# Optimization experiments

Hardware: AMD Instinct MI355X
Metric: run time of the kernel (lower is better)

## Reference

```python
import jax, jax.numpy as jnp
import numpy as np

B, N, D = 32, 4096, 256      # batch, num input features, input dim
S, H, M = 11, 256, 512       # num_slots, slot_size, mlp_hidden_size
ITERS = 3
ATTN_EPS = 1e-8
LN_EPS = 1e-5


def layer_norm(x, scale, offset):
    mu = jnp.mean(x, axis=-1, keepdims=True)
    var = jnp.var(x, axis=-1, keepdims=True)
    return (x - mu) * scale * jax.lax.rsqrt(var + LN_EPS) + offset


def gru_unroll(updates, w_i, w_h, b):
    # haiku hk.GRU unrolled over axis 1 (time_major=False), zero initial state.
    # updates: [B, T, H]
    h0 = jnp.zeros((updates.shape[0], H), updates.dtype)
    def step(h, x):
        gx = jnp.matmul(x, w_i)                                    # [B, 3H]
        zr = jax.nn.sigmoid(gx[:, :2 * H] + jnp.matmul(h, w_h[:, :2 * H]) + b[:2 * H])
        z, r = zr[:, :H], zr[:, H:]
        a = jnp.tanh(gx[:, 2 * H:] + jnp.matmul(r * h, w_h[:, 2 * H:]) + b[2 * H:])
        h_new = (1.0 - z) * h + z * a
        return h_new, h_new
    _, outs = jax.lax.scan(step, h0, jnp.swapaxes(updates, 0, 1))
    return jnp.swapaxes(outs, 0, 1)                                # [B, T, H]


def setup_inputs():
    key = jax.random.key(0)
    k = jax.random.split(key, 16)
    def lin(kk, fan_in, fan_out):
        return jax.random.normal(kk, (fan_in, fan_out), jnp.float32) / np.sqrt(fan_in).astype(np.float32)
    return {
        "inputs": jax.random.normal(k[0], (B, N, D), jnp.float32),
        "slot_noise": jax.random.normal(k[1], (B, S, H), jnp.float32),
        "ln_in_scale": jnp.ones((D,), jnp.float32),
        "ln_in_offset": jnp.zeros((D,), jnp.float32),
        "ln_slots_scale": jnp.ones((H,), jnp.float32),
        "ln_slots_offset": jnp.zeros((H,), jnp.float32),
        "ln_mlp_scale": jnp.ones((H,), jnp.float32),
        "ln_mlp_offset": jnp.zeros((H,), jnp.float32),
        "slots_mu": jax.random.normal(k[2], (1, 1, H), jnp.float32) * 0.1,
        "slots_log_sigma": jax.random.normal(k[3], (1, 1, H), jnp.float32) * 0.1 - 1.0,
        "Wq": lin(k[4], H, H),
        "Wk": lin(k[5], D, H),
        "Wv": lin(k[6], D, H),
        "gru_wi": lin(k[7], H, 3 * H),
        "gru_wh": lin(k[8], H, 3 * H),
        "gru_b": jnp.zeros((3 * H,), jnp.float32),
        "mlp_w1": lin(k[9], H, M),
        "mlp_b1": jnp.zeros((M,), jnp.float32),
        "mlp_w2": lin(k[10], M, H),
        "mlp_b2": jnp.zeros((H,), jnp.float32),
    }


def reference(inputs, slot_noise, ln_in_scale, ln_in_offset, ln_slots_scale,
              ln_slots_offset, ln_mlp_scale, ln_mlp_offset, slots_mu,
              slots_log_sigma, Wq, Wk, Wv, gru_wi, gru_wh, gru_b,
              mlp_w1, mlp_b1, mlp_w2, mlp_b2):
    x = layer_norm(inputs, ln_in_scale, ln_in_offset)
    kf = jnp.matmul(x, Wk)                                          # [B, N, H]
    vf = jnp.matmul(x, Wv)                                          # [B, N, H]
    slots = slots_mu + jnp.exp(slots_log_sigma) * slot_noise        # [B, S, H]
    scale = H ** (-0.5)
    for _ in range(ITERS):
        q = jnp.matmul(layer_norm(slots, ln_slots_scale, ln_slots_offset), Wq) * scale
        attn_logits = jnp.einsum('bnh,bsh->bns', kf, q)             # [B, N, S]
        attn = jax.nn.softmax(attn_logits, axis=-1) + ATTN_EPS      # softmax over slots
        attn = attn / jnp.sum(attn, axis=-2, keepdims=True)         # normalize over inputs
        updates = jnp.einsum('bns,bnh->bsh', attn, vf)              # [B, S, H]
        slots = gru_unroll(updates, gru_wi, gru_wh, gru_b)          # GRU over slot axis
        mlp_in = layer_norm(slots, ln_mlp_scale, ln_mlp_offset)
        hid = jax.nn.relu(jnp.matmul(mlp_in, mlp_w1) + mlp_b1)
        slots = slots + jnp.matmul(hid, mlp_w2) + mlp_b2
    return slots
```

## Files before the change

kernel.cpp:

```cpp
#include <hip/hip_runtime.h>

typedef unsigned short u16;
typedef __bf16 bf16x8 __attribute__((ext_vector_type(8)));
typedef float  f32x4  __attribute__((ext_vector_type(4)));
typedef unsigned short u16x8 __attribute__((ext_vector_type(8)));

union U8cast { u16x8 u; bf16x8 b; };

#define NB 32
#define NN 4096
#define ND 256
#define NS 11
#define NH 256
#define NM 512

__device__ __forceinline__ u16 f2bf(float f) {
  unsigned u = __float_as_uint(f);
  u += 0x7FFF + ((u >> 16) & 1);
  return (u16)(u >> 16);
}
__device__ __forceinline__ float bf2f(u16 h) {
  return __uint_as_float(((unsigned)h) << 16);
}

__device__ __forceinline__ void gload_lds16(const void* g, void* l) {
  __builtin_amdgcn_global_load_lds((const __attribute__((address_space(1))) void*)g,
                                   (__attribute__((address_space(3))) void*)l, 16, 0, 0);
}

__global__ void k_stats_ln(const float* __restrict__ x, const float* __restrict__ sc,
                           const float* __restrict__ of, u16* __restrict__ xbf) {
  int lane = threadIdx.x & 63;
  int wid  = threadIdx.x >> 6;
  int row  = blockIdx.x * 4 + wid;
  float4 v = *(const float4*)(x + (size_t)row * 256 + lane * 4);
  float s1 = v.x + v.y + v.z + v.w;
  float s2 = v.x*v.x + v.y*v.y + v.z*v.z + v.w*v.w;
#pragma unroll
  for (int off = 32; off; off >>= 1) { s1 += __shfl_xor(s1, off); s2 += __shfl_xor(s2, off); }
  float mu = s1 * (1.f/256.f);
  float rs = rsqrtf(s2 * (1.f/256.f) - mu*mu + 1e-5f);
  float4 s4 = *(const float4*)(sc + lane * 4);
  float4 o4 = *(const float4*)(of + lane * 4);
  ushort4 o;
  o.x = f2bf((v.x - mu) * (rs * s4.x) + o4.x);
  o.y = f2bf((v.y - mu) * (rs * s4.y) + o4.y);
  o.z = f2bf((v.z - mu) * (rs * s4.z) + o4.z);
  o.w = f2bf((v.w - mu) * (rs * s4.w) + o4.w);
  *(ushort4*)(xbf + (size_t)row * 256 + lane * 4) = o;
}

__global__ __launch_bounds__(256)
void k_cvt_w(const float* __restrict__ Wk, const float* __restrict__ Wv,
             u16* __restrict__ wT) {
  __shared__ float Lt[64][65];
  int bx = blockIdx.x;
  int kt = bx & 3, ct = bx >> 2;
  int k0 = kt * 64, c0 = ct * 64;
  const float* src = (c0 < 256) ? Wk : Wv;
  int c0m = c0 & 255;
  int t = threadIdx.x;
  int kr = t >> 2, part = t & 3;
  const float* sp = src + (size_t)(k0 + kr) * 256 + c0m + part * 16;
#pragma unroll
  for (int g = 0; g < 4; ++g) {
    float4 v = *(const float4*)(sp + g * 4);
    Lt[kr][part*16 + g*4 + 0] = v.x;
    Lt[kr][part*16 + g*4 + 1] = v.y;
    Lt[kr][part*16 + g*4 + 2] = v.z;
    Lt[kr][part*16 + g*4 + 3] = v.w;
  }
  __syncthreads();
  int cr = t >> 2;
  u16* wp = wT + (size_t)(c0 + cr) * 256 + k0 + part * 16;
#pragma unroll
  for (int g = 0; g < 2; ++g) {
    u16x8 o;
#pragma unroll
    for (int j = 0; j < 8; ++j) o[j] = f2bf(Lt[part*16 + g*8 + j][cr]);
    *(u16x8*)(wp + g * 8) = o;
  }
}

__global__ __launch_bounds__(256)
void k_mk(const float* __restrict__ Wq, const u16* __restrict__ wT,
          u16* __restrict__ Mb) {
  __shared__ float xn[256];
  __shared__ float part[8][256];
  int e = blockIdx.x, t = threadIdx.x;
  xn[t] = Wq[e*256 + t];
  __syncthreads();
  int tc = t & 31, kg = t >> 5;
  float a[8] = {};
#pragma unroll 8
  for (int kk = 0; kk < 32; ++kk) {
    int k = kg*32 + kk;
    float xv = xn[k];
    u16x8 wv = *(const u16x8*)(wT + k*256 + tc*8);
#pragma unroll
    for (int j = 0; j < 8; ++j) a[j] += xv * bf2f(wv[j]);
  }
  *(float4*)&part[kg][tc*8]     = make_float4(a[0], a[1], a[2], a[3]);
  *(float4*)&part[kg][tc*8 + 4] = make_float4(a[4], a[5], a[6], a[7]);
  __syncthreads();
  float s = 0.f;
#pragma unroll
  for (int g = 0; g < 8; ++g) s += part[g][t];
  Mb[e*256 + t] = f2bf(s);
}

__global__ void k_cvt_all(const float* __restrict__ wi, const float* __restrict__ wh,
                          const float* __restrict__ w1, const float* __restrict__ w2,
                          const float* __restrict__ noise, const float* __restrict__ smu,
                          const float* __restrict__ sls,
                          u16* __restrict__ wib, u16* __restrict__ whb,
                          u16* __restrict__ w1b, u16* __restrict__ w2b,
                          float* __restrict__ slots) {
  int idx = blockIdx.x * 256 + threadIdx.x;
  if      (idx < 196608) wib[idx]          = f2bf(wi[idx]);
  else if (idx < 393216) whb[idx - 196608] = f2bf(wh[idx - 196608]);
  else if (idx < 524288) w1b[idx - 393216] = f2bf(w1[idx - 393216]);
  else if (idx < 655360) w2b[idx - 524288] = f2bf(w2[idx - 524288]);
  else {
    int i = idx - 655360;
    int c = i & 255;
    slots[i] = smu[c] + expf(sls[c]) * noise[i];
  }
}

__global__ __launch_bounds__(256)
void k_gemm_vf(const u16* __restrict__ xbf, const u16* __restrict__ wTv,
               u16* __restrict__ vf) {
  __shared__ __align__(16) u16 Al[2][128 * 64];
  __shared__ __align__(16) u16 Bl[2][128 * 64];
  int t = threadIdx.x;
  int bid = blockIdx.x;
  int xcd  = bid & 7;
  int slot = bid >> 3;
  int colt = slot & 1;
  int rowt = xcd * 128 + (slot >> 1);
  int row0 = rowt * 128;
  int col0 = colt * 128;

  int lane = t & 63, w = t >> 6;
  int wm = (w & 1) * 64, wn = (w >> 1) * 64;
  int fr = lane & 15, kq = lane >> 4;

  int srow = w * 8 + (lane >> 3);
  int k2   = (((lane & 7) ^ ((lane >> 3) & 7)) << 4);
  const u16* agp = xbf + (size_t)(row0 + srow) * 256 + (k2 >> 1);
  const u16* bgp = wTv + (size_t)(col0 + srow) * 256 + (k2 >> 1);

  f32x4 acc[4][4] = {};

#define STAGE_VF(buf, kc)                                              \
  {                                                                    \
    u16* Aw = &Al[buf][w * 512];                                       \
    u16* Bw = &Bl[buf][w * 512];                                       \
    _Pragma("unroll")                                                  \
    for (int i = 0; i < 4; ++i) {                                      \
      gload_lds16(agp + (size_t)i * 32 * 256 + (kc), Aw + i * 2048);   \
      gload_lds16(bgp + (size_t)i * 32 * 256 + (kc), Bw + i * 2048);   \
    }                                                                  \
  }

  STAGE_VF(0, 0);
  __syncthreads();
#pragma unroll
  for (int t4 = 0; t4 < 4; ++t4) {
    if (t4 < 3) STAGE_VF((t4 + 1) & 1, (t4 + 1) * 64);
    const u16* Ab = Al[t4 & 1];
    const u16* Bb = Bl[t4 & 1];
#pragma unroll
    for (int ks = 0; ks < 2; ++ks) {
      int kb = ks * 64 + kq * 16;
      bf16x8 af[4], bfr[4];
#pragma unroll
      for (int i = 0; i < 4; ++i) {
        int row = wm + i * 16 + fr;
        af[i] = *(const bf16x8*)((const char*)Ab + row * 128 + (kb ^ ((fr & 7) << 4)));
      }
#pragma unroll
      for (int i = 0; i < 4; ++i) {
        int row = wn + i * 16 + fr;
        bfr[i] = *(const bf16x8*)((const char*)Bb + row * 128 + (kb ^ ((fr & 7) << 4)));
      }
#pragma unroll
      for (int im = 0; im < 4; ++im)
#pragma unroll
        for (int in = 0; in < 4; ++in)
          acc[im][in] = __builtin_amdgcn_mfma_f32_16x16x32_bf16(af[im], bfr[in], acc[im][in], 0, 0, 0);
    }
    __syncthreads();
  }
#undef STAGE_VF

  int r4 = kq * 4;
#pragma unroll
  for (int im = 0; im < 4; ++im)
#pragma unroll
    for (int in = 0; in < 4; ++in) {
      int gcol = col0 + wn + in*16 + fr;
#pragma unroll
      for (int r = 0; r < 4; ++r) {
        int grow = row0 + wm + im*16 + r4 + r;
        vf[(size_t)grow * 256 + gcol] = f2bf(acc[im][in][r]);
      }
    }
}

__global__ __launch_bounds__(256)
void k_q_ln(const float* __restrict__ slots, const float* __restrict__ sc,
            const float* __restrict__ of, const u16* __restrict__ Mb,
            float* __restrict__ qk2, float* __restrict__ updates,
            float* __restrict__ colsum) {
  __shared__ float xn[256];
  __shared__ float red[8];
  __shared__ float part[8][256];
  int row = blockIdx.x, t = threadIdx.x;
  float v = slots[row*256 + t];
  float s1 = v, s2 = v*v;
#pragma unroll
  for (int off = 32; off; off >>= 1) { s1 += __shfl_xor(s1, off); s2 += __shfl_xor(s2, off); }
  int w = t >> 6;
  if ((t & 63) == 0) { red[w*2] = s1; red[w*2+1] = s2; }
  __syncthreads();
  float a1 = red[0] + red[2] + red[4] + red[6];
  float a2 = red[1] + red[3] + red[5] + red[7];
  float mu = a1 * (1.f/256.f);
  float rs = rsqrtf(a2 * (1.f/256.f) - mu*mu + 1e-5f);
  xn[t] = (v - mu) * rs * sc[t] + of[t];
  updates[row*256 + t] = 0.f;
  if (t == 0) colsum[(row/11)*16 + (row%11)] = 0.f;
  __syncthreads();
  int tc = t & 31, kg = t >> 5;
  float a[8] = {};
#pragma unroll 8
  for (int kk = 0; kk < 32; ++kk) {
    int k = kg*32 + kk;
    float xv = xn[k];
    u16x8 wv = *(const u16x8*)(Mb + k*256 + tc*8);
#pragma unroll
    for (int j = 0; j < 8; ++j) a[j] += xv * bf2f(wv[j]);
  }
  *(float4*)&part[kg][tc*8]     = make_float4(a[0], a[1], a[2], a[3]);
  *(float4*)&part[kg][tc*8 + 4] = make_float4(a[4], a[5], a[6], a[7]);
  __syncthreads();
  float s = 0.f;
#pragma unroll
  for (int g = 0; g < 8; ++g) s += part[g][t];
  qk2[row*256 + t] = s * 0.0625f;
}

__global__ __launch_bounds__(256)
void k_attn_up(const u16* __restrict__ xbf, const u16* __restrict__ vf,
               const float* __restrict__ qg,
               float* __restrict__ updates, float* __restrict__ colsum) {
  __shared__ __align__(16) u16 kfL[64][264];
  __shared__ __align__(16) u16 vfL[64][256];
  __shared__ __align__(16) u16 qTL[16][264];
  __shared__ __align__(16) u16 PTL[16][72];
  __shared__ float Lg[64][17];
  int t = threadIdx.x;
  int b = blockIdx.y;
  int nb0 = blockIdx.x * 256;
  int lane = t & 63, w = t >> 6;
  int fr = lane & 15, kq = lane >> 4;

#pragma unroll
  for (int i = t; i < 512; i += 256) {
    int s = i >> 5, k0 = (i & 31) * 8;
    u16x8 o;
    if (s < 11) {
      const float* qp = qg + (size_t)b*2816 + s*256 + k0;
#pragma unroll
      for (int j = 0; j < 8; ++j) o[j] = f2bf(qp[j]);
    } else {
#pragma unroll
      for (int j = 0; j < 8; ++j) o[j] = 0;
    }
    *(u16x8*)&qTL[s][k0] = o;
  }
  for (int i = t; i < 16*72; i += 256) ((u16*)PTL)[i] = 0;

  f32x4 accU[4] = {};
  float csA[11];
#pragma unroll
  for (int s = 0; s < 11; ++s) csA[s] = 0.f;

  for (int c = 0; c < 4; ++c) {
    int n0 = nb0 + c*64;
    __syncthreads();
    {
      int hc = (t & 31) * 8;
#pragma unroll
      for (int nr = 0; nr < 8; ++nr) {
        int n = nr*8 + (t >> 5);
        size_t base = ((size_t)b*4096 + n0 + n) * 256;
        u16x8 kvk = *(const u16x8*)(xbf + base + hc);
        *(u16x8*)&kfL[n][hc] = kvk;
        u16x8 kvv = *(const u16x8*)(vf + base + hc);
        *(u16x8*)&vfL[n][hc ^ (((n >> 3) & 3) * 16)] = kvv;
      }
    }
    __syncthreads();
    {
      f32x4 aL = {};
#pragma unroll
      for (int kc = 0; kc < 256; kc += 32) {
        bf16x8 af = *(const bf16x8*)&kfL[w*16 + fr][kc + kq*8];
        bf16x8 bq = *(const bf16x8*)&qTL[fr][kc + kq*8];
        aL = __builtin_amdgcn_mfma_f32_16x16x32_bf16(af, bq, aL, 0, 0, 0);
      }
#pragma unroll
      for (int r = 0; r < 4; ++r)
        Lg[w*16 + kq*4 + r][fr] = aL[r];
    }
    __syncthreads();
    if (t < 64) {
      float p[11];
#pragma unroll
      for (int s = 0; s < 11; ++s) p[s] = Lg[t][s];
      float m = p[0];
#pragma unroll
      for (int s = 1; s < 11; ++s) m = fmaxf(m, p[s]);
      float Z = 0.f;
#pragma unroll
      for (int s = 0; s < 11; ++s) { p[s] = __expf(p[s] - m); Z += p[s]; }
      float iz = 1.f / Z;
#pragma unroll
      for (int s = 0; s < 11; ++s) {
        u16 pb = f2bf(p[s]*iz + 1e-8f);
        csA[s] += bf2f(pb);
        PTL[s][t] = pb;
      }
    }
    __syncthreads();
#pragma unroll
    for (int ht = 0; ht < 4; ++ht) {
      int h = w*64 + ht*16 + fr;
#pragma unroll
      for (int kc = 0; kc < 64; kc += 32) {
        bf16x8 aP = *(const bf16x8*)&PTL[fr][kc + kq*8];
        U8cast bv;
#pragma unroll
        for (int j = 0; j < 8; ++j) {
          int k = kc + kq*8 + j;
          bv.u[j] = vfL[k][h ^ (((k >> 3) & 3) * 16)];
        }
        accU[ht] = __builtin_amdgcn_mfma_f32_16x16x32_bf16(aP, bv.b, accU[ht], 0, 0, 0);
      }
    }
  }
#pragma unroll
  for (int ht = 0; ht < 4; ++ht) {
    int h = w*64 + ht*16 + fr;
#pragma unroll
    for (int r = 0; r < 4; ++r) {
      int s = kq*4 + r;
      if (s < 11)
        atomicAdd(&updates[((size_t)b*11 + s)*256 + h], accU[ht][r]);
    }
  }
  if (t < 64) {
#pragma unroll
    for (int s = 0; s < 11; ++s) {
#pragma unroll
      for (int off = 32; off; off >>= 1) csA[s] += __shfl_xor(csA[s], off);
    }
    if (lane == 0) {
#pragma unroll
      for (int s = 0; s < 11; ++s) atomicAdd(&colsum[b*16 + s], csA[s]);
    }
  }
}

__global__ __launch_bounds__(384)
void k_gx(const float* __restrict__ updates, const float* __restrict__ colsum,
          const u16* __restrict__ wib, float* __restrict__ gx) {
  __shared__ float xn[256];
  __shared__ float part[4][768];
  int row = blockIdx.x, t = threadIdx.x;
  if (t < 256) {
    float inv = 1.f / colsum[(row/11)*16 + (row%11)];
    xn[t] = updates[row*256 + t] * inv;
  }
  __syncthreads();
  int tc = t % 96, kg = t / 96;
  float a[8] = {};
#pragma unroll 4
  for (int kk = 0; kk < 64; ++kk) {
    int k = kg*64 + kk;
    float xv = xn[k];
    u16x8 wv = *(const u16x8*)(wib + k*768 + tc*8);
#pragma unroll
    for (int j = 0; j < 8; ++j) a[j] += xv * bf2f(wv[j]);
  }
  *(float4*)&part[kg][tc*8]     = make_float4(a[0], a[1], a[2], a[3]);
  *(float4*)&part[kg][tc*8 + 4] = make_float4(a[4], a[5], a[6], a[7]);
  __syncthreads();
#pragma unroll
  for (int c = t; c < 768; c += 384) {
    float s = part[0][c] + part[1][c] + part[2][c] + part[3][c];
    gx[row*768 + c] = s;
  }
}

__global__ __launch_bounds__(512)
void k_gru(const float* __restrict__ gx, const u16* __restrict__ whb,
           const float* __restrict__ gb, float* __restrict__ slots) {
  __shared__ float h[256], rh[256], zv[256];
  __shared__ float part[4096];
  int b = blockIdx.x, t = threadIdx.x;
  if (t < 256) h[t] = 0.f;
  __syncthreads();
  for (int step = 0; step < 11; ++step) {
    int row = b*11 + step;
    {
      int tc = t & 63, kg = t >> 6;
      float a[8] = {};
#pragma unroll 8
      for (int kk = 0; kk < 32; ++kk) {
        int k = kg*32 + kk;
        float xv = h[k];
        u16x8 wv = *(const u16x8*)(whb + k*768 + tc*8);
#pragma unroll
        for (int j = 0; j < 8; ++j) a[j] += xv * bf2f(wv[j]);
      }
      *(float4*)&part[kg*512 + tc*8]     = make_float4(a[0], a[1], a[2], a[3]);
      *(float4*)&part[kg*512 + tc*8 + 4] = make_float4(a[4], a[5], a[6], a[7]);
    }
    __syncthreads();
    {
      int c = t;
      float s = gx[row*768 + c] + gb[c];
#pragma unroll
      for (int g = 0; g < 8; ++g) s += part[g*512 + c];
      float sg = 1.f / (1.f + __expf(-s));
      if (c < 256) zv[c] = sg;
      else         rh[c - 256] = sg * h[c - 256];
    }
    __syncthreads();
    {
      int tc = t & 31, kg = t >> 5;
      float a[8] = {};
#pragma unroll 8
      for (int kk = 0; kk < 16; ++kk) {
        int k = kg*16 + kk;
        float xv = rh[k];
        u16x8 wv = *(const u16x8*)(whb + k*768 + 512 + tc*8);
#pragma unroll
        for (int j = 0; j < 8; ++j) a[j] += xv * bf2f(wv[j]);
      }
      *(float4*)&part[kg*256 + tc*8]     = make_float4(a[0], a[1], a[2], a[3]);
      *(float4*)&part[kg*256 + tc*8 + 4] = make_float4(a[4], a[5], a[6], a[7]);
    }
    __syncthreads();
    if (t < 256) {
      int c = t;
      float s = gx[row*768 + 512 + c] + gb[512 + c];
#pragma unroll
      for (int g = 0; g < 16; ++g) s += part[g*256 + c];
      float av = tanhf(s);
      float hn = (1.f - zv[c])*h[c] + zv[c]*av;
      h[c] = hn;
      slots[row*256 + c] = hn;
    }
    __syncthreads();
  }
}

__global__ __launch_bounds__(256)
void k_mlp(float* __restrict__ slots, const float* __restrict__ sc,
           const float* __restrict__ of, const u16* __restrict__ w1b,
           const float* __restrict__ b1, const u16* __restrict__ w2b,
           const float* __restrict__ b2, float* __restrict__ out2) {
  __shared__ float xn[256];
  __shared__ float hid[512];
  __shared__ float red[8];
  __shared__ float part[2048];
  int row = blockIdx.x, t = threadIdx.x;
  float v = slots[row*256 + t];
  float s1 = v, s2 = v*v;
#pragma unroll
  for (int off = 32; off; off >>= 1) { s1 += __shfl_xor(s1, off); s2 += __shfl_xor(s2, off); }
  int w = t >> 6;
  if ((t & 63) == 0) { red[w*2] = s1; red[w*2+1] = s2; }
  __syncthreads();
  float a1s = red[0] + red[2] + red[4] + red[6];
  float a2s = red[1] + red[3] + red[5] + red[7];
  float mu = a1s * (1.f/256.f);
  float rs = rsqrtf(a2s * (1.f/256.f) - mu*mu + 1e-5f);
  xn[t] = (v - mu) * rs * sc[t] + of[t];
  __syncthreads();
  {
    int tc = t & 63, kg = t >> 6;
    float a[8] = {};
#pragma unroll 4
    for (int kk = 0; kk < 64; ++kk) {
      int k = kg*64 + kk;
      float xv = xn[k];
      u16x8 wv = *(const u16x8*)(w1b + k*512 + tc*8);
#pragma unroll
      for (int j = 0; j < 8; ++j) a[j] += xv * bf2f(wv[j]);
    }
    *(float4*)&part[kg*512 + tc*8]     = make_float4(a[0], a[1], a[2], a[3]);
    *(float4*)&part[kg*512 + tc*8 + 4] = make_float4(a[4], a[5], a[6], a[7]);
  }
  __syncthreads();
#pragma unroll
  for (int c = t; c < 512; c += 256) {
    float s = b1[c];
#pragma unroll
    for (int g = 0; g < 4; ++g) s += part[g*512 + c];
    hid[c] = fmaxf(s, 0.f);
  }
  __syncthreads();
  {
    int tc = t & 31, kg = t >> 5;
    float a[8] = {};
#pragma unroll 4
    for (int kk = 0; kk < 64; ++kk) {
      int k = kg*64 + kk;
      float xv = hid[k];
      u16x8 wv = *(const u16x8*)(w2b + k*256 + tc*8);
#pragma unroll
      for (int j = 0; j < 8; ++j) a[j] += xv * bf2f(wv[j]);
    }
    *(float4*)&part[kg*256 + tc*8]     = make_float4(a[0], a[1], a[2], a[3]);
    *(float4*)&part[kg*256 + tc*8 + 4] = make_float4(a[4], a[5], a[6], a[7]);
  }
  __syncthreads();
  {
    float s = v + b2[t];
#pragma unroll
    for (int g = 0; g < 8; ++g) s += part[g*256 + t];
    slots[row*256 + t] = s;
    if (out2) out2[row*256 + t] = s;
  }
}

extern "C" void kernel_launch(void* const* d_in, const int* in_sizes, int n_in,
                              void* d_out, int out_size, void* d_ws, size_t ws_size,
                              hipStream_t stream) {
  (void)in_sizes; (void)n_in; (void)out_size; (void)ws_size;
  const float* inputs = (const float*)d_in[0];
  const float* noise  = (const float*)d_in[1];
  const float* lnin_s = (const float*)d_in[2];
  const float* lnin_o = (const float*)d_in[3];
  const float* lnsl_s = (const float*)d_in[4];
  const float* lnsl_o = (const float*)d_in[5];
  const float* lnml_s = (const float*)d_in[6];
  const float* lnml_o = (const float*)d_in[7];
  const float* smu    = (const float*)d_in[8];
  const float* sls    = (const float*)d_in[9];
  const float* Wq     = (const float*)d_in[10];
  const float* Wk     = (const float*)d_in[11];
  const float* Wv     = (const float*)d_in[12];
  const float* gwi    = (const float*)d_in[13];
  const float* gwh    = (const float*)d_in[14];
  const float* gb     = (const float*)d_in[15];
  const float* w1     = (const float*)d_in[16];
  const float* b1     = (const float*)d_in[17];
  const float* w2     = (const float*)d_in[18];
  const float* b2     = (const float*)d_in[19];

  char* ws = (char*)d_ws;
  u16*    vf      = (u16*)(ws);
  u16*    wT      = (u16*)(ws + 134217728);
  float*  slots   = (float*)(ws + 139984896);
  float*  updates = (float*)(ws + 140345344);
  float*  gx      = (float*)(ws + 140705792);
  float*  qk2     = (float*)(ws + 140705792);
  float*  colsum  = (float*)(ws + 141787136);
  u16*    Mb      = (u16*)(ws + 141789184);
  u16*    wib     = (u16*)(ws + 141920256);
  u16*    whb     = (u16*)(ws + 142313472);
  u16*    w1b     = (u16*)(ws + 142706688);
  u16*    w2b     = (u16*)(ws + 142968832);
  u16*    xbf     = (u16*)(ws + 143230976);

  k_stats_ln <<<32768, 256, 0, stream>>>(inputs, lnin_s, lnin_o, xbf);
  k_cvt_w    <<<32,    256, 0, stream>>>(Wk, Wv, wT);
  k_mk       <<<256,   256, 0, stream>>>(Wq, wT, Mb);
  k_cvt_all  <<<2912,  256, 0, stream>>>(gwi, gwh, w1, w2, noise, smu, sls,
                                         wib, whb, w1b, w2b, slots);
  k_gemm_vf  <<<2048,  256, 0, stream>>>(xbf, wT + 65536, vf);

  for (int it = 0; it < 3; ++it) {
    k_q_ln    <<<352, 256, 0, stream>>>(slots, lnsl_s, lnsl_o, Mb, qk2, updates, colsum);
    k_attn_up <<<dim3(16, 32), 256, 0, stream>>>(xbf, vf, qk2, updates, colsum);
    k_gx      <<<352, 384, 0, stream>>>(updates, colsum, wib, gx);
    k_gru     <<<32,  512, 0, stream>>>(gx, whb, gb, slots);
    k_mlp     <<<352, 256, 0, stream>>>(slots, lnml_s, lnml_o, w1b, b1, w2b, b2,
                                        (it == 2) ? (float*)d_out : nullptr);
  }
}
```

Measured before the change: 585.5 us.

## Fold Wv into GRU input weights and drop the value-projection GEMM

Uses associativity: updates·Wi = (attn^T·x)·Wv·Wi, so the value projection is folded into a precomputed Wv·Wi matrix (256x768, bf16). The attention kernel then aggregates normalized inputs directly instead of loading a separate vf tensor. This removes the large [B,N,H] GEMM and its 64MB write plus per-iteration reads. In exchange there is a small one-time 256x256x768 fp32 product, and the changed bf16 rounding order may shift numerics slightly.

```diff
diff --git a/kernel.cpp b/kernel.cpp
--- a/kernel.cpp
+++ b/kernel.cpp
@@ -21,11 +21,6 @@
 }
 __device__ __forceinline__ float bf2f(u16 h) {
   return __uint_as_float(((unsigned)h) << 16);
-}
-
-__device__ __forceinline__ void gload_lds16(const void* g, void* l) {
-  __builtin_amdgcn_global_load_lds((const __attribute__((address_space(1))) void*)g,
-                                   (__attribute__((address_space(3))) void*)l, 16, 0, 0);
 }
 
 __global__ void k_stats_ln(const float* __restrict__ x, const float* __restrict__ sc,
@@ -51,17 +46,14 @@
 }
 
 __global__ __launch_bounds__(256)
-void k_cvt_w(const float* __restrict__ Wk, const float* __restrict__ Wv,
-             u16* __restrict__ wT) {
+void k_cvt_w(const float* __restrict__ Wk, u16* __restrict__ wT) {
   __shared__ float Lt[64][65];
   int bx = blockIdx.x;
   int kt = bx & 3, ct = bx >> 2;
   int k0 = kt * 64, c0 = ct * 64;
-  const float* src = (c0 < 256) ? Wk : Wv;
-  int c0m = c0 & 255;
   int t = threadIdx.x;
   int kr = t >> 2, part = t & 3;
-  const float* sp = src + (size_t)(k0 + kr) * 256 + c0m + part * 16;
+  const float* sp = Wk + (size_t)(k0 + kr) * 256 + c0 + part * 16;
 #pragma unroll
   for (int g = 0; g < 4; ++g) {
     float4 v = *(const float4*)(sp + g * 4);
@@ -109,104 +101,50 @@
   Mb[e*256 + t] = f2bf(s);
 }
 
-__global__ void k_cvt_all(const float* __restrict__ wi, const float* __restrict__ wh,
-                          const float* __restrict__ w1, const float* __restrict__ w2,
+__global__ __launch_bounds__(384)
+void k_wvi(const float* __restrict__ Wv, const float* __restrict__ wi,
+           u16* __restrict__ wvib) {
+  __shared__ float xn[256];
+  __shared__ float part[4][768];
+  int d = blockIdx.x, t = threadIdx.x;
+  if (t < 256) xn[t] = Wv[d*256 + t];
+  __syncthreads();
+  int tc = t % 96, kg = t / 96;
+  float a[8] = {};
+#pragma unroll 4
+  for (int kk = 0; kk < 64; ++kk) {
+    int k = kg*64 + kk;
+    float xv = xn[k];
+    float4 w0 = *(const float4*)(wi + (size_t)k*768 + tc*8);
+    float4 w1 = *(const float4*)(wi + (size_t)k*768 + tc*8 + 4);
+    a[0] += xv * w0.x; a[1] += xv * w0.y; a[2] += xv * w0.z; a[3] += xv * w0.w;
+    a[4] += xv * w1.x; a[5] += xv * w1.y; a[6] += xv * w1.z; a[7] += xv * w1.w;
+  }
+  *(float4*)&part[kg][tc*8]     = make_float4(a[0], a[1], a[2], a[3]);
+  *(float4*)&part[kg][tc*8 + 4] = make_float4(a[4], a[5], a[6], a[7]);
+  __syncthreads();
+#pragma unroll
+  for (int c = t; c < 768; c += 384) {
+    float s = part[0][c] + part[1][c] + part[2][c] + part[3][c];
+    wvib[d*768 + c] = f2bf(s);
+  }
+}
+
+__global__ void k_cvt_all(const float* __restrict__ wh, const float* __restrict__ w1,
+                          const float* __restrict__ w2,
                           const float* __restrict__ noise, const float* __restrict__ smu,
                           const float* __restrict__ sls,
-                          u16* __restrict__ wib, u16* __restrict__ whb,
-                          u16* __restrict__ w1b, u16* __restrict__ w2b,
-                          float* __restrict__ slots) {
+                          u16* __restrict__ whb, u16* __restrict__ w1b,
+                          u16* __restrict__ w2b, float* __restrict__ slots) {
   int idx = blockIdx.x * 256 + threadIdx.x;
-  if      (idx < 196608) wib[idx]          = f2bf(wi[idx]);
-  else if (idx < 393216) whb[idx - 196608] = f2bf(wh[idx - 196608]);
-  else if (idx < 524288) w1b[idx - 393216] = f2bf(w1[idx - 393216]);
-  else if (idx < 655360) w2b[idx - 524288] = f2bf(w2[idx - 524288]);
+  if      (idx < 196608) whb[idx]          = f2bf(wh[idx]);
+  else if (idx < 327680) w1b[idx - 196608] = f2bf(w1[idx - 196608]);
+  else if (idx < 458752) w2b[idx - 327680] = f2bf(w2[idx - 327680]);
   else {
-    int i = idx - 655360;
+    int i = idx - 458752;
     int c = i & 255;
     slots[i] = smu[c] + expf(sls[c]) * noise[i];
   }
-}
-
-__global__ __launch_bounds__(256)
-void k_gemm_vf(const u16* __restrict__ xbf, const u16* __restrict__ wTv,
-               u16* __restrict__ vf) {
-  __shared__ __align__(16) u16 Al[2][128 * 64];
-  __shared__ __align__(16) u16 Bl[2][128 * 64];
-  int t = threadIdx.x;
-  int bid = blockIdx.x;
-  int xcd  = bid & 7;
-  int slot = bid >> 3;
-  int colt = slot & 1;
-  int rowt = xcd * 128 + (slot >> 1);
-  int row0 = rowt * 128;
-  int col0 = colt * 128;
-
-  int lane = t & 63, w = t >> 6;
-  int wm = (w & 1) * 64, wn = (w >> 1) * 64;
-  int fr = lane & 15, kq = lane >> 4;
-
-  int srow = w * 8 + (lane >> 3);
-  int k2   = (((lane & 7) ^ ((lane >> 3) & 7)) << 4);
-  const u16* agp = xbf + (size_t)(row0 + srow) * 256 + (k2 >> 1);
-  const u16* bgp = wTv + (size_t)(col0 + srow) * 256 + (k2 >> 1);
-
-  f32x4 acc[4][4] = {};
-
-#define STAGE_VF(buf, kc)                                              \
-  {                                                                    \
-    u16* Aw = &Al[buf][w * 512];                                       \
-    u16* Bw = &Bl[buf][w * 512];                                       \
-    _Pragma("unroll")                                                  \
-    for (int i = 0; i < 4; ++i) {                                      \
-      gload_lds16(agp + (size_t)i * 32 * 256 + (kc), Aw + i * 2048);   \
-      gload_lds16(bgp + (size_t)i * 32 * 256 + (kc), Bw + i * 2048);   \
-    }                                                                  \
-  }
-
-  STAGE_VF(0, 0);
-  __syncthreads();
-#pragma unroll
-  for (int t4 = 0; t4 < 4; ++t4) {
-    if (t4 < 3) STAGE_VF((t4 + 1) & 1, (t4 + 1) * 64);
-    const u16* Ab = Al[t4 & 1];
-    const u16* Bb = Bl[t4 & 1];
-#pragma unroll
-    for (int ks = 0; ks < 2; ++ks) {
-      int kb = ks * 64 + kq * 16;
-      bf16x8 af[4], bfr[4];
-#pragma unroll
-      for (int i = 0; i < 4; ++i) {
-        int row = wm + i * 16 + fr;
-        af[i] = *(const bf16x8*)((const char*)Ab + row * 128 + (kb ^ ((fr & 7) << 4)));
-      }
-#pragma unroll
-      for (int i = 0; i < 4; ++i) {
-        int row = wn + i * 16 + fr;
-        bfr[i] = *(const bf16x8*)((const char*)Bb + row * 128 + (kb ^ ((fr & 7) << 4)));
-      }
-#pragma unroll
-      for (int im = 0; im < 4; ++im)
-#pragma unroll
-        for (int in = 0; in < 4; ++in)
-          acc[im][in] = __builtin_amdgcn_mfma_f32_16x16x32_bf16(af[im], bfr[in], acc[im][in], 0, 0, 0);
-    }
-    __syncthreads();
-  }
-#undef STAGE_VF
-
-  int r4 = kq * 4;
-#pragma unroll
-  for (int im = 0; im < 4; ++im)
-#pragma unroll
-    for (int in = 0; in < 4; ++in) {
-      int gcol = col0 + wn + in*16 + fr;
-#pragma unroll
-      for (int r = 0; r < 4; ++r) {
-        int grow = row0 + wm + im*16 + r4 + r;
-        vf[(size_t)grow * 256 + gcol] = f2bf(acc[im][in][r]);
-      }
-    }
 }
 
 __global__ __launch_bounds__(256)
@@ -253,8 +191,7 @@
 }
 
 __global__ __launch_bounds__(256)
-void k_attn_up(const u16* __restrict__ xbf, const u16* __restrict__ vf,
-               const float* __restrict__ qg,
+void k_attn_up(const u16* __restrict__ xbf, const float* __restrict__ qg,
                float* __restrict__ updates, float* __restrict__ colsum) {
   __shared__ __align__(16) u16 kfL[64][264];
   __shared__ __align__(16) u16 vfL[64][256];
@@ -299,8 +236,7 @@
         size_t base = ((size_t)b*4096 + n0 + n) * 256;
         u16x8 kvk = *(const u16x8*)(xbf + base + hc);
         *(u16x8*)&kfL[n][hc] = kvk;
-        u16x8 kvv = *(const u16x8*)(vf + base + hc);
-        *(u16x8*)&vfL[n][hc ^ (((n >> 3) & 3) * 16)] = kvv;
+        *(u16x8*)&vfL[n][hc ^ (((n >> 3) & 3) * 16)] = kvk;
       }
     }
     __syncthreads();
@@ -377,7 +313,7 @@
 
 __global__ __launch_bounds__(384)
 void k_gx(const float* __restrict__ updates, const float* __restrict__ colsum,
-          const u16* __restrict__ wib, float* __restrict__ gx) {
+          const u16* __restrict__ wvib, float* __restrict__ gx) {
   __shared__ float xn[256];
   __shared__ float part[4][768];
   int row = blockIdx.x, t = threadIdx.x;
@@ -392,7 +328,7 @@
   for (int kk = 0; kk < 64; ++kk) {
     int k = kg*64 + kk;
     float xv = xn[k];
-    u16x8 wv = *(const u16x8*)(wib + k*768 + tc*8);
+    u16x8 wv = *(const u16x8*)(wvib + k*768 + tc*8);
 #pragma unroll
     for (int j = 0; j < 8; ++j) a[j] += xv * bf2f(wv[j]);
   }
@@ -566,7 +502,6 @@
   const float* b2     = (const float*)d_in[19];
 
   char* ws = (char*)d_ws;
-  u16*    vf      = (u16*)(ws);
   u16*    wT      = (u16*)(ws + 134217728);
   float*  slots   = (float*)(ws + 139984896);
   float*  updates = (float*)(ws + 140345344);
@@ -574,23 +509,23 @@
   float*  qk2     = (float*)(ws + 140705792);
   float*  colsum  = (float*)(ws + 141787136);
   u16*    Mb      = (u16*)(ws + 141789184);
-  u16*    wib     = (u16*)(ws + 141920256);
+  u16*    wvib    = (u16*)(ws + 141920256);
   u16*    whb     = (u16*)(ws + 142313472);
   u16*    w1b     = (u16*)(ws + 142706688);
   u16*    w2b     = (u16*)(ws + 142968832);
   u16*    xbf     = (u16*)(ws + 143230976);
 
   k_stats_ln <<<32768, 256, 0, stream>>>(inputs, lnin_s, lnin_o, xbf);
-  k_cvt_w    <<<32,    256, 0, stream>>>(Wk, Wv, wT);
+  k_cvt_w    <<<16,    256, 0, stream>>>(Wk, wT);
   k_mk       <<<256,   256, 0, stream>>>(Wq, wT, Mb);
-  k_cvt_all  <<<2912,  256, 0, stream>>>(gwi, gwh, w1, w2, noise, smu, sls,
-                                         wib, whb, w1b, w2b, slots);
-  k_gemm_vf  <<<2048,  256, 0, stream>>>(xbf, wT + 65536, vf);
+  k_wvi      <<<256,   384, 0, stream>>>(Wv, gwi, wvib);
+  k_cvt_all  <<<2144,  256, 0, stream>>>(gwh, w1, w2, noise, smu, sls,
+                                         whb, w1b, w2b, slots);
 
   for (int it = 0; it < 3; ++it) {
     k_q_ln    <<<352, 256, 0, stream>>>(slots, lnsl_s, lnsl_o, Mb, qk2, updates, colsum);
-    k_attn_up <<<dim3(16, 32), 256, 0, stream>>>(xbf, vf, qk2, updates, colsum);
-    k_gx      <<<352, 384, 0, stream>>>(updates, colsum, wib, gx);
+    k_attn_up <<<dim3(16, 32), 256, 0, stream>>>(xbf, qk2, updates, colsum);
+    k_gx      <<<352, 384, 0, stream>>>(updates, colsum, wvib, gx);
     k_gru     <<<32,  512, 0, stream>>>(gx, whb, gb, slots);
     k_mlp     <<<352, 256, 0, stream>>>(slots, lnml_s, lnml_o, w1b, b1, w2b, b2,
                                         (it == 2) ? (float*)d_out : nullptr);
```

Measured after the change: 548.4 us. -6.3%, faster.
